# Kernel optimization log

Measured on AMD Instinct MI355X. Metric: run time of the kernel, lower is better.

Reference implementation:

```python
import jax, jax.numpy as jnp
import numpy as np

N = 8192            # n_nodes
E = 262144          # n_edges (avg degree 32)
IN_F, HID_F, OUT_F = 256, 128, 64


def _xavier(key, shape):
    fan_out, fan_in = shape
    lim = np.sqrt(6.0 / (fan_in + fan_out))
    return jax.random.uniform(key, shape, jnp.float32, -lim, lim)


def setup_inputs() -> dict:
    key = jax.random.key(0)
    k = jax.random.split(key, 7)
    edge_src = jnp.sort(jax.random.randint(k[0], (E,), 0, N))
    edge_dst = jax.random.randint(k[1], (E,), 0, N)
    h = jax.random.normal(k[2], (N, IN_F), jnp.float32)
    W0 = _xavier(k[3], (HID_F, IN_F))
    Wmu = _xavier(k[4], (OUT_F, HID_F))
    Wls = _xavier(k[5], (OUT_F, HID_F)) * 0.1  # keep exp(log_sigma) tame
    eps = jax.random.normal(k[6], (N, OUT_F), jnp.float32)
    return {"h": h, "W0": W0, "Wmu": Wmu, "Wls": Wls, "eps": eps,
            "edge_src": edge_src, "edge_dst": edge_dst}


def _gcn(edge_src, edge_dst, h, W, act=None):
    # a is the unweighted sparse adjacency given by (edge_src -> row, edge_dst -> col)
    n = h.shape[0]
    deg = jax.ops.segment_sum(jnp.ones(edge_src.shape[0], h.dtype), edge_src,
                              num_segments=n)                    # row-sum of a
    norm = jnp.clip(deg, 1.0, None) ** -0.5                      # d^{-1/2}, clamp(min=1)
    h = h * norm[:, None]                                        # pre-norm
    h = h @ W.T                                                  # Linear (no bias)
    h = jax.ops.segment_sum(h[edge_dst], edge_src, num_segments=n)  # a @ h (SpMM)
    h = h * norm[:, None]                                        # post-norm
    if act is not None:
        h = act(h)
    return h


def reference(h, W0, Wmu, Wls, eps, edge_src, edge_dst):
    h1 = _gcn(edge_src, edge_dst, h, W0, jax.nn.relu)            # gcn0 + ReLU
    mu = _gcn(edge_src, edge_dst, h1, Wmu)                       # gcn_mu
    log_sigma = _gcn(edge_src, edge_dst, h1, Wls)                # gcn_log_sigma
    z = mu + jnp.exp(log_sigma) * eps                            # q_z.rsample()
    logits = z @ z.T                                             # Bernoulli logits [N, N]
    return logits
```

## Files before the change

### kernel.cpp

```cpp
#include <hip/hip_runtime.h>
#include <hip/hip_bf16.h>
#include <cstdint>
#include <cstddef>

#define NN 8192
#define IN_F 256
#define HID_F 128
#define OUT_F 64

typedef __attribute__((ext_vector_type(8))) short short8v;
typedef __attribute__((ext_vector_type(4))) float f32x4;
typedef __attribute__((ext_vector_type(4))) unsigned short ushort4v;

static __device__ __forceinline__ unsigned short f2bf(float x) {
    unsigned int u = __float_as_uint(x);
    unsigned int r = (u + 0x7fffu + ((u >> 16) & 1u)) >> 16;
    return (unsigned short)r;
}
static __device__ __forceinline__ float bf2f(unsigned short u) {
    return __uint_as_float(((unsigned int)u) << 16);
}

__global__ void k_rowptr(const int* __restrict__ src, int* __restrict__ rp, int E, int N) {
    int i = blockIdx.x * blockDim.x + threadIdx.x;
    if (i >= E) return;
    int s = src[i];
    int p = (i == 0) ? -1 : src[i - 1];
    for (int n = p + 1; n <= s; ++n) rp[n] = i;
    if (i == E - 1) {
        for (int n = s + 1; n <= N; ++n) rp[n] = E;
    }
}

__global__ void k_norm(const int* __restrict__ rp, float* __restrict__ norm, int N) {
    int n = blockIdx.x * blockDim.x + threadIdx.x;
    if (n >= N) return;
    int d = rp[n + 1] - rp[n];
    float df = (float)(d < 1 ? 1 : d);
    norm[n] = rsqrtf(df);
}

__global__ void k_conv_h(const float* __restrict__ h, const float* __restrict__ norm,
                         unsigned short* __restrict__ hi, unsigned short* __restrict__ lo,
                         int total4) {
    int i = blockIdx.x * blockDim.x + threadIdx.x;
    if (i >= total4) return;
    int n = i / (IN_F / 4);
    float nv = norm[n];
    float4 v = reinterpret_cast<const float4*>(h)[i];
    ushort4v h4, l4;
    float x;
    x = v.x * nv; h4.x = f2bf(x); l4.x = f2bf(x - bf2f(h4.x));
    x = v.y * nv; h4.y = f2bf(x); l4.y = f2bf(x - bf2f(h4.y));
    x = v.z * nv; h4.z = f2bf(x); l4.z = f2bf(x - bf2f(h4.z));
    x = v.w * nv; h4.w = f2bf(x); l4.w = f2bf(x - bf2f(h4.w));
    reinterpret_cast<ushort4v*>(hi)[i] = h4;
    reinterpret_cast<ushort4v*>(lo)[i] = l4;
}

__global__ void k_conv_w(const float* __restrict__ W0, const float* __restrict__ Wmu,
                         const float* __restrict__ Wls,
                         unsigned short* __restrict__ W0h, unsigned short* __restrict__ W0l,
                         unsigned short* __restrict__ Wch, unsigned short* __restrict__ Wcl) {
    int i = blockIdx.x * blockDim.x + threadIdx.x;
    const int n0 = HID_F * IN_F;
    const int n1 = 2 * OUT_F * HID_F;
    if (i < n0) {
        float x = W0[i];
        unsigned short hh = f2bf(x);
        W0h[i] = hh; W0l[i] = f2bf(x - bf2f(hh));
    } else if (i < n0 + n1) {
        int j = i - n0;
        int r = j / HID_F, c = j % HID_F;
        float x = (r < OUT_F) ? Wmu[r * HID_F + c] : Wls[(r - OUT_F) * HID_F + c];
        unsigned short hh = f2bf(x);
        Wch[j] = hh; Wcl[j] = f2bf(x - bf2f(hh));
    }
}

template <int K, int MT, int NT>
__global__ __launch_bounds__(256) void k_gemm_bt(
    const unsigned short* __restrict__ Ahi, const unsigned short* __restrict__ Alo,
    const unsigned short* __restrict__ Bhi, const unsigned short* __restrict__ Blo,
    float* __restrict__ C, int ldc) {
    const int lane = threadIdx.x & 63;
    const int wid = threadIdx.x >> 6;
    const int wr = wid >> 1, wc = wid & 1;
    const long i0 = (long)blockIdx.x * (32 * MT) + wr * (16 * MT);
    const long j0 = (long)blockIdx.y * (32 * NT) + wc * (16 * NT);
    const int rl = lane & 15;
    const int kq = lane >> 4;

    f32x4 acc[MT][NT] = {};

    for (int kc = 0; kc < K; kc += 32) {
        const int kb = kc + kq * 8;
        short8v ah[MT], al[MT], bh[NT], bl[NT];
#pragma unroll
        for (int m = 0; m < MT; ++m) {
            size_t off = (size_t)(i0 + m * 16 + rl) * K + kb;
            ah[m] = *reinterpret_cast<const short8v*>(Ahi + off);
            al[m] = *reinterpret_cast<const short8v*>(Alo + off);
        }
#pragma unroll
        for (int n = 0; n < NT; ++n) {
            size_t off = (size_t)(j0 + n * 16 + rl) * K + kb;
            bh[n] = *reinterpret_cast<const short8v*>(Bhi + off);
            bl[n] = *reinterpret_cast<const short8v*>(Blo + off);
        }
#pragma unroll
        for (int m = 0; m < MT; ++m) {
#pragma unroll
            for (int n = 0; n < NT; ++n) {
                acc[m][n] = __builtin_amdgcn_mfma_f32_16x16x32_bf16(ah[m], bh[n], acc[m][n], 0, 0, 0);
                acc[m][n] = __builtin_amdgcn_mfma_f32_16x16x32_bf16(ah[m], bl[n], acc[m][n], 0, 0, 0);
                acc[m][n] = __builtin_amdgcn_mfma_f32_16x16x32_bf16(al[m], bh[n], acc[m][n], 0, 0, 0);
            }
        }
    }

    const int crow = (lane >> 4) * 4;
#pragma unroll
    for (int m = 0; m < MT; ++m) {
#pragma unroll
        for (int n = 0; n < NT; ++n) {
            size_t base = (size_t)(i0 + m * 16 + crow) * ldc + (size_t)(j0 + n * 16 + rl);
#pragma unroll
            for (int r = 0; r < 4; ++r)
                C[base + (size_t)r * ldc] = acc[m][n][r];
        }
    }
}

__global__ __launch_bounds__(128) void k_spmm1(
    const float* __restrict__ X, const int* __restrict__ rp, const int* __restrict__ dst,
    const float* __restrict__ norm, float* __restrict__ h1p) {
    int n = blockIdx.x;
    int t = threadIdx.x;
    int e0 = rp[n], e1 = rp[n + 1];
    float acc = 0.f;
    int e = e0;
    for (; e + 4 <= e1; e += 4) {
        int d0 = dst[e] * HID_F, d1 = dst[e + 1] * HID_F;
        int d2 = dst[e + 2] * HID_F, d3 = dst[e + 3] * HID_F;
        acc += X[d0 + t];
        acc += X[d1 + t];
        acc += X[d2 + t];
        acc += X[d3 + t];
    }
    for (; e < e1; ++e) acc += X[dst[e] * HID_F + t];
    float nv = norm[n];
    float v = acc * nv;
    v = v > 0.f ? v : 0.f;
    h1p[n * HID_F + t] = v * nv;
}

__global__ __launch_bounds__(128) void k_spmm2(
    const float* __restrict__ X, const int* __restrict__ rp, const int* __restrict__ dst,
    unsigned short* __restrict__ hi, unsigned short* __restrict__ lo) {
    int n = blockIdx.x;
    int t = threadIdx.x;
    int e0 = rp[n], e1 = rp[n + 1];
    float acc = 0.f;
    int e = e0;
    for (; e + 4 <= e1; e += 4) {
        int d0 = dst[e] * HID_F, d1 = dst[e + 1] * HID_F;
        int d2 = dst[e + 2] * HID_F, d3 = dst[e + 3] * HID_F;
        acc += X[d0 + t];
        acc += X[d1 + t];
        acc += X[d2 + t];
        acc += X[d3 + t];
    }
    for (; e < e1; ++e) acc += X[dst[e] * HID_F + t];
    unsigned short hh = f2bf(acc);
    hi[n * HID_F + t] = hh;
    lo[n * HID_F + t] = f2bf(acc - bf2f(hh));
}

__global__ void k_z(const float* __restrict__ P, const float* __restrict__ norm,
                    const float* __restrict__ eps,
                    unsigned short* __restrict__ zh, unsigned short* __restrict__ zl) {
    int i = blockIdx.x * blockDim.x + threadIdx.x;
    if (i >= NN * OUT_F) return;
    int n = i >> 6, f = i & 63;
    float nv = norm[n];
    float mu = P[n * HID_F + f] * nv;
    float ls = P[n * HID_F + 64 + f] * nv;
    float z = mu + expf(ls) * eps[i];
    unsigned short hh = f2bf(z);
    zh[i] = hh;
    zl[i] = f2bf(z - bf2f(hh));
}

extern "C" void kernel_launch(void* const* d_in, const int* in_sizes, int n_in,
                              void* d_out, int out_size, void* d_ws, size_t ws_size,
                              hipStream_t stream) {
    const float* h   = (const float*)d_in[0];
    const float* W0  = (const float*)d_in[1];
    const float* Wmu = (const float*)d_in[2];
    const float* Wls = (const float*)d_in[3];
    const float* eps = (const float*)d_in[4];
    const int* esrc  = (const int*)d_in[5];
    const int* edst  = (const int*)d_in[6];
    const int E = in_sizes[5];
    const int N = NN;

    char* w = (char*)d_ws;
    auto alloc = [&](size_t bytes) {
        char* p = w;
        w += (bytes + 511) & ~(size_t)511;
        return p;
    };
    int* rp             = (int*)alloc((N + 1) * sizeof(int));
    float* norm         = (float*)alloc(N * sizeof(float));
    unsigned short* Hh  = (unsigned short*)alloc((size_t)N * IN_F * 2);
    unsigned short* Hl  = (unsigned short*)alloc((size_t)N * IN_F * 2);
    unsigned short* W0h = (unsigned short*)alloc(HID_F * IN_F * 2);
    unsigned short* W0l = (unsigned short*)alloc(HID_F * IN_F * 2);
    unsigned short* Wch = (unsigned short*)alloc(2 * OUT_F * HID_F * 2);
    unsigned short* Wcl = (unsigned short*)alloc(2 * OUT_F * HID_F * 2);
    float* X1           = (float*)alloc((size_t)N * HID_F * sizeof(float));
    float* h1p          = (float*)alloc((size_t)N * HID_F * sizeof(float));
    unsigned short* Agh = (unsigned short*)alloc((size_t)N * HID_F * 2);
    unsigned short* Agl = (unsigned short*)alloc((size_t)N * HID_F * 2);
    float* P            = (float*)alloc((size_t)N * HID_F * sizeof(float));
    unsigned short* Zh  = (unsigned short*)alloc((size_t)N * OUT_F * 2);
    unsigned short* Zl  = (unsigned short*)alloc((size_t)N * OUT_F * 2);

    k_rowptr<<<(E + 255) / 256, 256, 0, stream>>>(esrc, rp, E, N);
    k_norm<<<(N + 255) / 256, 256, 0, stream>>>(rp, norm, N);
    k_conv_h<<<((N * IN_F / 4) + 255) / 256, 256, 0, stream>>>(h, norm, Hh, Hl, N * IN_F / 4);
    k_conv_w<<<(HID_F * IN_F + 2 * OUT_F * HID_F + 255) / 256, 256, 0, stream>>>(
        W0, Wmu, Wls, W0h, W0l, Wch, Wcl);

    k_gemm_bt<IN_F, 2, 2><<<dim3(N / 64, HID_F / 64), 256, 0, stream>>>(
        Hh, Hl, W0h, W0l, X1, HID_F);

    k_spmm1<<<N, 128, 0, stream>>>(X1, rp, edst, norm, h1p);
    k_spmm2<<<N, 128, 0, stream>>>(h1p, rp, edst, Agh, Agl);

    k_gemm_bt<HID_F, 2, 2><<<dim3(N / 64, HID_F / 64), 256, 0, stream>>>(
        Agh, Agl, Wch, Wcl, P, HID_F);

    k_z<<<((N * OUT_F) + 255) / 256, 256, 0, stream>>>(P, norm, eps, Zh, Zl);

    k_gemm_bt<OUT_F, 4, 4><<<dim3(N / 128, N / 128), 256, 0, stream>>>(
        Zh, Zl, Zh, Zl, (float*)d_out, N);
}
```

Before: 137.8 us.

## Fuse graph prep kernels and fold z sampling into second GEMM epilogue

Merges the row-pointer, degree-norm and weight conversion kernels into one prep kernel, which finds row pointers by binary search over the sorted edge sources. The second GEMM now keeps its output tile in shared memory and computes the reparameterised z directly in the epilogue, so the fp32 P buffer and the separate k_z launch are gone. This cuts launch count and a full N×128 fp32 round trip through global memory. The cost is binary-search work per node and a GEMM grid of only N/64 blocks.

```diff
diff --git a/kernel.cpp b/kernel.cpp
--- a/kernel.cpp
+++ b/kernel.cpp
@@ -4,6 +4,7 @@
 #include <cstddef>
 
 #define NN 8192
+#define EE 262144
 #define IN_F 256
 #define HID_F 128
 #define OUT_F 64
@@ -21,23 +22,41 @@
     return __uint_as_float(((unsigned int)u) << 16);
 }
 
-__global__ void k_rowptr(const int* __restrict__ src, int* __restrict__ rp, int E, int N) {
+__global__ void k_prep(const int* __restrict__ src,
+                       const float* __restrict__ W0, const float* __restrict__ Wmu,
+                       const float* __restrict__ Wls,
+                       int* __restrict__ rp, float* __restrict__ norm,
+                       unsigned short* __restrict__ W0h, unsigned short* __restrict__ W0l,
+                       unsigned short* __restrict__ Wch, unsigned short* __restrict__ Wcl) {
     int i = blockIdx.x * blockDim.x + threadIdx.x;
-    if (i >= E) return;
-    int s = src[i];
-    int p = (i == 0) ? -1 : src[i - 1];
-    for (int n = p + 1; n <= s; ++n) rp[n] = i;
-    if (i == E - 1) {
-        for (int n = s + 1; n <= N; ++n) rp[n] = E;
-    }
-}
-
-__global__ void k_norm(const int* __restrict__ rp, float* __restrict__ norm, int N) {
-    int n = blockIdx.x * blockDim.x + threadIdx.x;
-    if (n >= N) return;
-    int d = rp[n + 1] - rp[n];
-    float df = (float)(d < 1 ? 1 : d);
-    norm[n] = rsqrtf(df);
+    if (i <= NN) {
+        auto lb = [&](int key) {
+            int lo = 0, hi = EE;
+            while (lo < hi) { int mid = (lo + hi) >> 1; if (src[mid] < key) lo = mid + 1; else hi = mid; }
+            return lo;
+        };
+        int a = lb(i);
+        rp[i] = a;
+        if (i < NN) {
+            int d = lb(i + 1) - a;
+            norm[i] = rsqrtf((float)(d < 1 ? 1 : d));
+        }
+    } else {
+        int j = i - (NN + 1);
+        const int n0 = HID_F * IN_F;
+        const int n1 = 2 * OUT_F * HID_F;
+        if (j < n0) {
+            float x = W0[j];
+            unsigned short hh = f2bf(x);
+            W0h[j] = hh; W0l[j] = f2bf(x - bf2f(hh));
+        } else if (j < n0 + n1) {
+            int q = j - n0;
+            int r = q / HID_F, c = q % HID_F;
+            float x = (r < OUT_F) ? Wmu[r * HID_F + c] : Wls[(r - OUT_F) * HID_F + c];
+            unsigned short hh = f2bf(x);
+            Wch[q] = hh; Wcl[q] = f2bf(x - bf2f(hh));
+        }
+    }
 }
 
 __global__ void k_conv_h(const float* __restrict__ h, const float* __restrict__ norm,
@@ -58,41 +77,17 @@
     reinterpret_cast<ushort4v*>(lo)[i] = l4;
 }
 
-__global__ void k_conv_w(const float* __restrict__ W0, const float* __restrict__ Wmu,
-                         const float* __restrict__ Wls,
-                         unsigned short* __restrict__ W0h, unsigned short* __restrict__ W0l,
-                         unsigned short* __restrict__ Wch, unsigned short* __restrict__ Wcl) {
-    int i = blockIdx.x * blockDim.x + threadIdx.x;
-    const int n0 = HID_F * IN_F;
-    const int n1 = 2 * OUT_F * HID_F;
-    if (i < n0) {
-        float x = W0[i];
-        unsigned short hh = f2bf(x);
-        W0h[i] = hh; W0l[i] = f2bf(x - bf2f(hh));
-    } else if (i < n0 + n1) {
-        int j = i - n0;
-        int r = j / HID_F, c = j % HID_F;
-        float x = (r < OUT_F) ? Wmu[r * HID_F + c] : Wls[(r - OUT_F) * HID_F + c];
-        unsigned short hh = f2bf(x);
-        Wch[j] = hh; Wcl[j] = f2bf(x - bf2f(hh));
-    }
-}
-
 template <int K, int MT, int NT>
 __global__ __launch_bounds__(256) void k_gemm_bt(
     const unsigned short* __restrict__ Ahi, const unsigned short* __restrict__ Alo,
     const unsigned short* __restrict__ Bhi, const unsigned short* __restrict__ Blo,
     float* __restrict__ C, int ldc) {
-    const int lane = threadIdx.x & 63;
-    const int wid = threadIdx.x >> 6;
+    const int lane = threadIdx.x & 63, wid = threadIdx.x >> 6;
     const int wr = wid >> 1, wc = wid & 1;
     const long i0 = (long)blockIdx.x * (32 * MT) + wr * (16 * MT);
     const long j0 = (long)blockIdx.y * (32 * NT) + wc * (16 * NT);
-    const int rl = lane & 15;
-    const int kq = lane >> 4;
-
+    const int rl = lane & 15, kq = lane >> 4;
     f32x4 acc[MT][NT] = {};
-
     for (int kc = 0; kc < K; kc += 32) {
         const int kb = kc + kq * 8;
         short8v ah[MT], al[MT], bh[NT], bl[NT];
@@ -109,19 +104,17 @@
             bl[n] = *reinterpret_cast<const short8v*>(Blo + off);
         }
 #pragma unroll
-        for (int m = 0; m < MT; ++m) {
+        for (int m = 0; m < MT; ++m)
 #pragma unroll
             for (int n = 0; n < NT; ++n) {
                 acc[m][n] = __builtin_amdgcn_mfma_f32_16x16x32_bf16(ah[m], bh[n], acc[m][n], 0, 0, 0);
                 acc[m][n] = __builtin_amdgcn_mfma_f32_16x16x32_bf16(ah[m], bl[n], acc[m][n], 0, 0, 0);
                 acc[m][n] = __builtin_amdgcn_mfma_f32_16x16x32_bf16(al[m], bh[n], acc[m][n], 0, 0, 0);
             }
-        }
-    }
-
+    }
     const int crow = (lane >> 4) * 4;
 #pragma unroll
-    for (int m = 0; m < MT; ++m) {
+    for (int m = 0; m < MT; ++m)
 #pragma unroll
         for (int n = 0; n < NT; ++n) {
             size_t base = (size_t)(i0 + m * 16 + crow) * ldc + (size_t)(j0 + n * 16 + rl);
@@ -129,7 +122,6 @@
             for (int r = 0; r < 4; ++r)
                 C[base + (size_t)r * ldc] = acc[m][n][r];
         }
-    }
 }
 
 __global__ __launch_bounds__(128) void k_spmm1(
@@ -177,19 +169,70 @@
     lo[n * HID_F + t] = f2bf(acc - bf2f(hh));
 }
 
-__global__ void k_z(const float* __restrict__ P, const float* __restrict__ norm,
-                    const float* __restrict__ eps,
-                    unsigned short* __restrict__ zh, unsigned short* __restrict__ zl) {
-    int i = blockIdx.x * blockDim.x + threadIdx.x;
-    if (i >= NN * OUT_F) return;
-    int n = i >> 6, f = i & 63;
-    float nv = norm[n];
-    float mu = P[n * HID_F + f] * nv;
-    float ls = P[n * HID_F + 64 + f] * nv;
-    float z = mu + expf(ls) * eps[i];
-    unsigned short hh = f2bf(z);
-    zh[i] = hh;
-    zl[i] = f2bf(z - bf2f(hh));
+__global__ __launch_bounds__(256) void k_gemm2z(
+    const unsigned short* __restrict__ Ah16, const unsigned short* __restrict__ Al16,
+    const unsigned short* __restrict__ Bh16, const unsigned short* __restrict__ Bl16,
+    const float* __restrict__ norm, const float* __restrict__ eps,
+    unsigned short* __restrict__ Zh, unsigned short* __restrict__ Zl) {
+    const int lane = threadIdx.x & 63, wid = threadIdx.x >> 6;
+    const int wr = wid >> 1, wc = wid & 1;
+    const int R0 = blockIdx.x * 64;
+    const int rl = lane & 15, kq = lane >> 4;
+    f32x4 acc[2][4] = {};
+    for (int kc = 0; kc < HID_F; kc += 32) {
+        const int kb = kc + kq * 8;
+        short8v ah[2], al[2], bh[4], bl[4];
+#pragma unroll
+        for (int m = 0; m < 2; ++m) {
+            size_t off = (size_t)(R0 + wr * 32 + m * 16 + rl) * HID_F + kb;
+            ah[m] = *reinterpret_cast<const short8v*>(Ah16 + off);
+            al[m] = *reinterpret_cast<const short8v*>(Al16 + off);
+        }
+#pragma unroll
+        for (int n = 0; n < 4; ++n) {
+            size_t off = (size_t)(wc * 64 + n * 16 + rl) * HID_F + kb;
+            bh[n] = *reinterpret_cast<const short8v*>(Bh16 + off);
+            bl[n] = *reinterpret_cast<const short8v*>(Bl16 + off);
+        }
+#pragma unroll
+        for (int m = 0; m < 2; ++m)
+#pragma unroll
+            for (int n = 0; n < 4; ++n) {
+                acc[m][n] = __builtin_amdgcn_mfma_f32_16x16x32_bf16(ah[m], bh[n], acc[m][n], 0, 0, 0);
+                acc[m][n] = __builtin_amdgcn_mfma_f32_16x16x32_bf16(ah[m], bl[n], acc[m][n], 0, 0, 0);
+                acc[m][n] = __builtin_amdgcn_mfma_f32_16x16x32_bf16(al[m], bh[n], acc[m][n], 0, 0, 0);
+            }
+    }
+    __shared__ __align__(16) float Pl[64][132];
+#pragma unroll
+    for (int m = 0; m < 2; ++m)
+#pragma unroll
+        for (int n = 0; n < 4; ++n)
+#pragma unroll
+            for (int r = 0; r < 4; ++r)
+                Pl[wr * 32 + m * 16 + 4 * kq + r][wc * 64 + n * 16 + rl] = acc[m][n][r];
+    __syncthreads();
+    const int fg = threadIdx.x & 15;
+    const int rr = threadIdx.x >> 4;
+#pragma unroll
+    for (int p = 0; p < 4; ++p) {
+        int rloc = p * 16 + rr;
+        int row = R0 + rloc;
+        float nv = norm[row];
+        f32x4 mu = *reinterpret_cast<const f32x4*>(&Pl[rloc][4 * fg]);
+        f32x4 ls = *reinterpret_cast<const f32x4*>(&Pl[rloc][64 + 4 * fg]);
+        f32x4 ev = *reinterpret_cast<const f32x4*>(eps + (size_t)row * OUT_F + 4 * fg);
+        ushort4v zh, zl;
+#pragma unroll
+        for (int q = 0; q < 4; ++q) {
+            float z = mu[q] * nv + expf(ls[q] * nv) * ev[q];
+            unsigned short hh = f2bf(z);
+            zh[q] = hh;
+            zl[q] = f2bf(z - bf2f(hh));
+        }
+        *reinterpret_cast<ushort4v*>(Zh + (size_t)row * OUT_F + 4 * fg) = zh;
+        *reinterpret_cast<ushort4v*>(Zl + (size_t)row * OUT_F + 4 * fg) = zl;
+    }
 }
 
 extern "C" void kernel_launch(void* const* d_in, const int* in_sizes, int n_in,
@@ -202,8 +245,6 @@
     const float* eps = (const float*)d_in[4];
     const int* esrc  = (const int*)d_in[5];
     const int* edst  = (const int*)d_in[6];
-    const int E = in_sizes[5];
-    const int N = NN;
 
     char* w = (char*)d_ws;
     auto alloc = [&](size_t bytes) {
@@ -211,39 +252,35 @@
         w += (bytes + 511) & ~(size_t)511;
         return p;
     };
-    int* rp             = (int*)alloc((N + 1) * sizeof(int));
-    float* norm         = (float*)alloc(N * sizeof(float));
-    unsigned short* Hh  = (unsigned short*)alloc((size_t)N * IN_F * 2);
-    unsigned short* Hl  = (unsigned short*)alloc((size_t)N * IN_F * 2);
+    int* rp             = (int*)alloc((NN + 1) * sizeof(int));
+    float* norm         = (float*)alloc(NN * sizeof(float));
     unsigned short* W0h = (unsigned short*)alloc(HID_F * IN_F * 2);
     unsigned short* W0l = (unsigned short*)alloc(HID_F * IN_F * 2);
     unsigned short* Wch = (unsigned short*)alloc(2 * OUT_F * HID_F * 2);
     unsigned short* Wcl = (unsigned short*)alloc(2 * OUT_F * HID_F * 2);
-    float* X1           = (float*)alloc((size_t)N * HID_F * sizeof(float));
-    float* h1p          = (float*)alloc((size_t)N * HID_F * sizeof(float));
-    unsigned short* Agh = (unsigned short*)alloc((size_t)N * HID_F * 2);
-    unsigned short* Agl = (unsigned short*)alloc((size_t)N * HID_F * 2);
-    float* P            = (float*)alloc((size_t)N * HID_F * sizeof(float));
-    unsigned short* Zh  = (unsigned short*)alloc((size_t)N * OUT_F * 2);
-    unsigned short* Zl  = (unsigned short*)alloc((size_t)N * OUT_F * 2);
-
-    k_rowptr<<<(E + 255) / 256, 256, 0, stream>>>(esrc, rp, E, N);
-    k_norm<<<(N + 255) / 256, 256, 0, stream>>>(rp, norm, N);
-    k_conv_h<<<((N * IN_F / 4) + 255) / 256, 256, 0, stream>>>(h, norm, Hh, Hl, N * IN_F / 4);
-    k_conv_w<<<(HID_F * IN_F + 2 * OUT_F * HID_F + 255) / 256, 256, 0, stream>>>(
-        W0, Wmu, Wls, W0h, W0l, Wch, Wcl);
-
-    k_gemm_bt<IN_F, 2, 2><<<dim3(N / 64, HID_F / 64), 256, 0, stream>>>(
+    unsigned short* Hh  = (unsigned short*)alloc((size_t)NN * IN_F * 2);
+    unsigned short* Hl  = (unsigned short*)alloc((size_t)NN * IN_F * 2);
+    float* X1           = (float*)alloc((size_t)NN * HID_F * sizeof(float));
+    float* h1p          = (float*)alloc((size_t)NN * HID_F * sizeof(float));
+    unsigned short* Agh = (unsigned short*)alloc((size_t)NN * HID_F * 2);
+    unsigned short* Agl = (unsigned short*)alloc((size_t)NN * HID_F * 2);
+    unsigned short* Zh  = (unsigned short*)alloc((size_t)NN * OUT_F * 2);
+    unsigned short* Zl  = (unsigned short*)alloc((size_t)NN * OUT_F * 2);
+
+    const int prep_threads = (NN + 1) + HID_F * IN_F + 2 * OUT_F * HID_F;
+    k_prep<<<(prep_threads + 255) / 256, 256, 0, stream>>>(
+        esrc, W0, Wmu, Wls, rp, norm, W0h, W0l, Wch, Wcl);
+
+    k_conv_h<<<((NN * IN_F / 4) + 255) / 256, 256, 0, stream>>>(h, norm, Hh, Hl, NN * IN_F / 4);
+
+    k_gemm_bt<IN_F, 2, 2><<<dim3(NN / 64, HID_F / 64), 256, 0, stream>>>(
         Hh, Hl, W0h, W0l, X1, HID_F);
 
-    k_spmm1<<<N, 128, 0, stream>>>(X1, rp, edst, norm, h1p);
-    k_spmm2<<<N, 128, 0, stream>>>(h1p, rp, edst, Agh, Agl);
-
-    k_gemm_bt<HID_F, 2, 2><<<dim3(N / 64, HID_F / 64), 256, 0, stream>>>(
-        Agh, Agl, Wch, Wcl, P, HID_F);
-
-    k_z<<<((N * OUT_F) + 255) / 256, 256, 0, stream>>>(P, norm, eps, Zh, Zl);
-
-    k_gemm_bt<OUT_F, 4, 4><<<dim3(N / 128, N / 128), 256, 0, stream>>>(
-        Zh, Zl, Zh, Zl, (float*)d_out, N);
-}
+    k_spmm1<<<NN, 128, 0, stream>>>(X1, rp, edst, norm, h1p);
+    k_spmm2<<<NN, 128, 0, stream>>>(h1p, rp, edst, Agh, Agl);
+
+    k_gemm2z<<<NN / 64, 256, 0, stream>>>(Agh, Agl, Wch, Wcl, norm, eps, Zh, Zl);
+
+    k_gemm_bt<OUT_F, 4, 4><<<dim3(NN / 128, NN / 128), 256, 0, stream>>>(
+        Zh, Zl, Zh, Zl, (float*)d_out, NN);
+}
```

Measured after the change: 141.1 us. 1.02x slower.
